# Performance work log

Measured on AMD Instinct MI355X. Metric: run time of the kernel, lower is better.

## Reference

```python
import jax, jax.numpy as jnp
import numpy as np

# ---- problem constants (match init_kwargs / input_specs) ----
R = 10          # rand_iter
B = 8           # num examples
NPG = 1024      # nodes per example (equal-sized groups)
M = 512         # centroids per group = fps_ratio(0.5) * NPG
TOL = 1e-3
MAX_ITER = 300
SCORE_NORM = 1  # L1 scoring


def setup_inputs() -> dict:
    key = jax.random.key(0)
    pos = jax.random.normal(key, (B * NPG, 3), dtype=jnp.float32)
    batch = (jnp.arange(B * NPG) // NPG).astype(jnp.int32)  # sorted example ids
    return {"pos": pos, "batch": batch}


def _fps(p, start):
    """Farthest point sampling on one group. p: [n,3] -> indices [M].
    torch_cluster.fps uses a random start; randomness across the R replicas
    comes from the start index."""
    n = p.shape[0]
    mind = jnp.full((n,), jnp.inf, dtype=p.dtype)

    def step(carry, _):
        mind, last = carry
        d = jnp.sum((p - p[last]) ** 2, axis=-1)     # [n]
        mind = jnp.minimum(mind, d)
        nxt = jnp.argmax(mind).astype(last.dtype)
        return (mind, nxt), last

    (_, _), idx = jax.lax.scan(step, (mind, start), None, length=M)
    return idx  # [M]


def _assign_update(p, c):
    """One k-means step for all groups. p: [g,n,3], c: [g,m,3].
    nearest-centroid assign (within group == within example) + scatter-mean
    update; empty clusters keep their old centroid (mask logic in torch src)."""
    p2 = jnp.sum(p * p, axis=-1)                                 # [g,n]
    c2 = jnp.sum(c * c, axis=-1)                                 # [g,m]
    d2 = p2[:, :, None] - 2.0 * jnp.einsum('gnd,gmd->gnm', p, c) + c2[:, None, :]
    cls = jnp.argmin(d2, axis=-1)                                # [g,n]
    seg = jax.vmap(lambda x, i: jax.ops.segment_sum(x, i, num_segments=M))
    sums = seg(p, cls)                                           # [g,m,3]
    cnts = seg(jnp.ones(p.shape[:2], p.dtype), cls)[..., None]   # [g,m,1]
    newc = jnp.where(cnts > 0, sums / jnp.maximum(cnts, 1.0), c)
    return newc, cls


def reference(pos, batch):
    # replicate data R times (SymmetricKMeans big_pos / big_batch)
    p = pos.reshape(B, NPG, 3)
    big = jnp.broadcast_to(p[None], (R, B, NPG, 3)).reshape(R * B, NPG, 3)

    # FPS init with a different random start per replica-group
    starts = jax.random.randint(jax.random.key(1), (R * B,), 0, NPG)
    idx = jax.vmap(_fps)(big, starts)                            # [g,M]
    cents = jnp.take_along_axis(big, idx[..., None], axis=1)     # [g,M,3]

    # k-means loop with convergence check (KMeans.forward)
    def cond(st):
        c, cls, done, i = st
        return (~done) & (i < MAX_ITER)

    def body(st):
        c, cls, done, i = st
        newc, cls = _assign_update(big, c)
        done = jnp.all(jnp.linalg.norm(c - newc, axis=-1) < TOL)
        return (newc, cls, done, i + 1)

    cls0 = jnp.zeros((R * B, NPG), jnp.int32)
    c, cls, _, _ = jax.lax.while_loop(
        cond, body, (cents, cls0, jnp.array(False), jnp.int32(0)))

    # score: L1 distance to assigned centroid, summed per example (score_norm=1)
    cvec = jnp.take_along_axis(c, cls[..., None], axis=1)        # [g,n,3]
    scores = jnp.sum(jnp.abs(big - cvec), axis=(-1, -2)).reshape(R, B)

    classification = cls.reshape(R, B * NPG)                     # per-group labels
    return classification, c, scores
```

## Files before the change

### kernel.cpp

```cpp
#include <hip/hip_runtime.h>
#include <math.h>


#define NGRP   80
#define NPTS   1024
#define NCTR   512
#define MAXIT  300
#define NTHR   1024
#define RING   64
#define LEAD   48
#define OUT_CENT  81920
#define OUT_SCORE 204800

typedef float v2f __attribute__((ext_vector_type(2)));
static __device__ __forceinline__ v2f mk2(float a, float b) {
  v2f r; r.x = a; r.y = b; return r;
}

__device__ float4   g_cent[NGRP * NCTR];
__device__ int      g_rcls[RING][NGRP * NPTS];
__device__ float4   g_rcent[RING][NGRP * NCTR];
__device__ unsigned g_conv32[MAXIT][32];
__device__ unsigned g_T[32];
__device__ unsigned g_water[32];

__device__ __forceinline__ void tf2x32(unsigned k0, unsigned k1,
                                       unsigned x0, unsigned x1,
                                       unsigned &o0, unsigned &o1) {
  unsigned ks2 = k0 ^ k1 ^ 0x1BD11BDAu;
#define RND(r) { x0 += x1; x1 = (x1 << (r)) | (x1 >> (32 - (r))); x1 ^= x0; }
  x0 += k0; x1 += k1;
  RND(13) RND(15) RND(26) RND(6)
  x0 += k1;  x1 += ks2 + 1u;
  RND(17) RND(29) RND(16) RND(24)
  x0 += ks2; x1 += k0 + 2u;
  RND(13) RND(15) RND(26) RND(6)
  x0 += k0;  x1 += k1 + 3u;
  RND(17) RND(29) RND(16) RND(24)
  x0 += k1;  x1 += ks2 + 4u;
  RND(13) RND(15) RND(26) RND(6)
  x0 += ks2; x1 += k0 + 5u;
#undef RND
  o0 = x0; o1 = x1;
}

#define DPP_MAXF(CTRL) asm volatile("s_nop 1\n\tv_max_f32 %0, %0, %0 " CTRL \
                                    : "+v"(bv));
#define DPP_MINU(CTRL) asm volatile("s_nop 1\n\tv_min_u32 %0, %0, %0 " CTRL \
                                    : "+v"(ci));

__device__ __forceinline__ int wave_iscan(int x) {
  x += __builtin_amdgcn_update_dpp(0, x, 0x111, 0xF, 0xF, true);
  x += __builtin_amdgcn_update_dpp(0, x, 0x112, 0xF, 0xF, true);
  x += __builtin_amdgcn_update_dpp(0, x, 0x114, 0xF, 0xF, true);
  x += __builtin_amdgcn_update_dpp(0, x, 0x118, 0xF, 0xF, true);
  x += __builtin_amdgcn_update_dpp(0, x, 0x142, 0xA, 0xF, true);
  x += __builtin_amdgcn_update_dpp(0, x, 0x143, 0xC, 0xF, true);
  return x;
}

__device__ __forceinline__ void conv_scan(unsigned w, bool &closed, bool &allc) {
  unsigned hz = 0u; bool ac = true;
#pragma unroll
  for (int i = 0; i < 20; ++i) {
    unsigned d = __hip_atomic_load(&g_conv32[w][i], __ATOMIC_RELAXED,
                                   __HIP_MEMORY_SCOPE_AGENT);
    hz |= (d - 0x01010101u) & ~d & 0x80808080u;
    ac = ac && (d == 0x02020202u);
  }
  closed = (hz == 0u); allc = ac;
}

__global__ __launch_bounds__(64) void fps_kernel(const float *__restrict__ pos) {
  const int g = blockIdx.x, t = threadIdx.x;
  const int e = g & 7;
  __shared__ float4 sp4[NPTS];
  {
    const int gid = g * 64 + t, stride = NGRP * 64;
    for (int k = gid; k < MAXIT * 32; k += stride) g_conv32[0][k] = 0u;
    if (gid == 0) { g_T[0] = 0u; g_water[0] = 0u; }
  }
  unsigned s0, s1, o0, o1;
  tf2x32(0u, 1u, 0u, 1u, s0, s1);
  tf2x32(s0, s1, 0u, (unsigned)g, o0, o1);
  int last = (int)((o0 ^ o1) & 1023u);

  const float *p = pos + (size_t)e * NPTS * 3;
  v2f xp[8], yp[8], zp[8], mdp[8];
#pragma unroll
  for (int q = 0; q < 8; ++q) {
    int n0 = (2 * q) * 64 + t, n1 = (2 * q + 1) * 64 + t;
    xp[q] = mk2(p[n0 * 3 + 0], p[n1 * 3 + 0]);
    yp[q] = mk2(p[n0 * 3 + 1], p[n1 * 3 + 1]);
    zp[q] = mk2(p[n0 * 3 + 2], p[n1 * 3 + 2]);
    sp4[n0] = make_float4(xp[q].x, yp[q].x, zp[q].x, 0.f);
    sp4[n1] = make_float4(xp[q].y, yp[q].y, zp[q].y, 0.f);
    mdp[q] = mk2(__int_as_float(0x7f800000), __int_as_float(0x7f800000));
  }
  __syncthreads();
  for (int j = 0; j < NCTR; ++j) {
    const float4 L = sp4[last];
    if (t == 0) {
      float c2 = __fadd_rn(__fadd_rn(__fmul_rn(L.x, L.x), __fmul_rn(L.y, L.y)),
                           __fmul_rn(L.z, L.z));
      g_cent[(size_t)g * NCTR + j] = make_float4(L.x, L.y, L.z, c2);
    }
    {
#pragma clang fp contract(off)
      const v2f lx2 = mk2(L.x, L.x), ly2 = mk2(L.y, L.y), lz2 = mk2(L.z, L.z);
#pragma unroll
      for (int q = 0; q < 8; ++q) {
        v2f dx = xp[q] - lx2, dy = yp[q] - ly2, dz = zp[q] - lz2;
        v2f d = (dx * dx + dy * dy) + dz * dz;
        mdp[q] = __builtin_elementwise_min(mdp[q], d);
      }
    }
    v2f m01 = __builtin_elementwise_max(mdp[0], mdp[1]);
    v2f m23 = __builtin_elementwise_max(mdp[2], mdp[3]);
    v2f m45 = __builtin_elementwise_max(mdp[4], mdp[5]);
    v2f m67 = __builtin_elementwise_max(mdp[6], mdp[7]);
    v2f m03 = __builtin_elementwise_max(m01, m23);
    v2f m47 = __builtin_elementwise_max(m45, m67);
    v2f m07 = __builtin_elementwise_max(m03, m47);
    float bv = fmaxf(m07.x, m07.y);
    DPP_MAXF("row_ror:1")
    DPP_MAXF("row_ror:2")
    DPP_MAXF("row_ror:4")
    DPP_MAXF("row_ror:8")
    DPP_MAXF("row_bcast:15 row_mask:0xa")
    DPP_MAXF("row_bcast:31 row_mask:0xc")
    asm volatile("s_nop 1");
    const float gmax = __int_as_float(
        __builtin_amdgcn_readlane(__float_as_int(bv), 63));

    unsigned cd[16];
#pragma unroll
    for (int k = 0; k < 16; ++k) {
      const float mv = (k & 1) ? mdp[k >> 1].y : mdp[k >> 1].x;
      cd[k] = (mv == gmax) ? (unsigned)(k * 64 + t) : 0x7fffffffu;
    }
#pragma unroll
    for (int s = 8; s >= 1; s >>= 1)
#pragma unroll
      for (int i = 0; i < s; ++i) cd[i] = cd[i] < cd[i + s] ? cd[i] : cd[i + s];
    unsigned ci = cd[0];
    DPP_MINU("row_ror:1")
    DPP_MINU("row_ror:2")
    DPP_MINU("row_ror:4")
    DPP_MINU("row_ror:8")
    DPP_MINU("row_bcast:15 row_mask:0xa")
    DPP_MINU("row_bcast:31 row_mask:0xc")
    asm volatile("s_nop 1");
    last = (int)__builtin_amdgcn_readlane((int)ci, 63);
  }
}

__global__ __launch_bounds__(NTHR) void kmeans_kernel(
    const float *__restrict__ pos, float *__restrict__ out) {
  const int g = blockIdx.x, t = threadIdx.x;
  const int e = g & 7;
  const int lane = t & 63, wv = t >> 6;

  __shared__ float  scp[NCTR / 2][8];
  __shared__ float  spx[NPTS], spy[NPTS], spz[NPTS];
  __shared__ int    slab[NPTS];
  __shared__ int    cnt[NCTR], offs[NCTR];
  __shared__ int    idx[NPTS];
  __shared__ float  redf[16];
  __shared__ double redd[4];
  __shared__ int    swtot[8];
  __shared__ unsigned s_ctl;

  const int cc7 = t & 127, cbid = (t >> 7) & 3;
  const int cq = cc7 + (cbid >> 1) * 128, cs = cbid & 1;

  {
    const float *gp = pos + (size_t)e * NPTS * 3;
    spx[t] = gp[t * 3 + 0]; spy[t] = gp[t * 3 + 1]; spz[t] = gp[t * 3 + 2];
    if (t < NCTR) {
      float4 cc = g_cent[(size_t)g * NCTR + t];
      scp[cq][0 + cs] = cc.x; scp[cq][2 + cs] = cc.y;
      scp[cq][4 + cs] = cc.z; scp[cq][6 + cs] = cc.w;
    }
    if (t == 0) s_ctl = 0u;
  }
  __syncthreads();

  const float px = spx[t], py = spy[t], pz = spz[t];
  const float p2 = __fadd_rn(__fadd_rn(__fmul_rn(px, px), __fmul_rn(py, py)),
                             __fmul_rn(pz, pz));
  const v2f px2 = mk2(px, px), py2 = mk2(py, py), pz2 = mk2(pz, pz);
  const v2f p22 = mk2(p2, p2), two2 = mk2(2.0f, 2.0f);

  int done_sT = -1;
  for (int it = 0; it < MAXIT; ++it) {
    float best0 = __int_as_float(0x7f800000), best1 = best0,
          best2 = best0, best3 = best0;
    int im0 = 0, im1 = 0, im2 = 0, im3 = 0;
    {
#pragma clang fp contract(off)
#pragma unroll 2
      for (int m = 0; m < NCTR / 4; ++m) {
        const float4 lo0 = *(const float4 *)&scp[m][0];
        const float4 hi0 = *(const float4 *)&scp[m][4];
        const float4 lo1 = *(const float4 *)&scp[m + 128][0];
        const float4 hi1 = *(const float4 *)&scp[m + 128][4];
        v2f t0 = px2 * mk2(lo0.x, lo0.y);
        t0 = __builtin_elementwise_fma(py2, mk2(lo0.z, lo0.w), t0);
        t0 = __builtin_elementwise_fma(pz2, mk2(hi0.x, hi0.y), t0);
        v2f dA = (p22 - two2 * t0) + mk2(hi0.z, hi0.w);
        v2f t1 = px2 * mk2(lo1.x, lo1.y);
        t1 = __builtin_elementwise_fma(py2, mk2(lo1.z, lo1.w), t1);
        t1 = __builtin_elementwise_fma(pz2, mk2(hi1.x, hi1.y), t1);
        v2f dB = (p22 - two2 * t1) + mk2(hi1.z, hi1.w);
        float d0 = dA.x, d1 = dA.y, d2 = dB.x, d3 = dB.y;
        if (d0 < best0) { best0 = d0; im0 = m; }
        if (d1 < best1) { best1 = d1; im1 = m; }
        if (d2 < best2) { best2 = d2; im2 = m; }
        if (d3 < best3) { best3 = d3; im3 = m; }
      }
    }
    float best = best0; int bm = im0;
    if (best1 < best) { best = best1; bm = 128 + im1; }
    if (best2 < best) { best = best2; bm = 256 + im2; }
    if (best3 < best) { best = best3; bm = 384 + im3; }
    const int slot = it & (RING - 1);
    g_rcls[slot][(size_t)g * NPTS + t] = bm;
    slab[t] = bm;
    if (t < NCTR) cnt[t] = 0;
    __syncthreads();

    {
      const unsigned tv = s_ctl;
      if (tv != 0u && (int)tv <= it) {
        done_sT = (int)tv - 1;
        break;
      }
    }

    atomicAdd(&cnt[slab[t]], 1);
    __syncthreads();
    int sc = 0;
    if (t < NCTR) {
      sc = wave_iscan(cnt[t]);
      if (lane == 63) swtot[wv] = sc;
    }
    __syncthreads();
    if (t < NCTR) {
      int pre = 0;
#pragma unroll
      for (int w = 0; w < 8; ++w) pre += (w < wv) ? swtot[w] : 0;
      offs[t] = sc + pre;
      cnt[t] = 0;
    }
    __syncthreads();
    {
      int c0 = slab[t]; int sl0 = atomicAdd(&cnt[c0], 1);
      idx[(c0 ? offs[c0 - 1] : 0) + sl0] = t;
    }
    __syncthreads();
    float mx = 0.0f;
    if (t < NCTR) {
      const int c = t;
      const int base = c ? offs[c - 1] : 0;
      const int kk = offs[c] - base;
      for (int i = base + 1; i < base + kk; ++i) {
        int v = idx[i], j = i - 1;
        while (j >= base && idx[j] > v) { idx[j + 1] = idx[j]; --j; }
        idx[j + 1] = v;
      }
      float4 oldc;
      oldc.x = scp[cq][0 + cs]; oldc.y = scp[cq][2 + cs];
      oldc.z = scp[cq][4 + cs]; oldc.w = scp[cq][6 + cs];
      float nx, ny, nz;
      if (kk > 0) {
        float sxx = 0.f, syy = 0.f, szz = 0.f;
        for (int i = 0; i < kk; ++i) {
          int n2 = idx[base + i];
          sxx = __fadd_rn(sxx, spx[n2]);
          syy = __fadd_rn(syy, spy[n2]);
          szz = __fadd_rn(szz, spz[n2]);
        }
        float fc = (float)kk;
        nx = __fdiv_rn(sxx, fc); ny = __fdiv_rn(syy, fc); nz = __fdiv_rn(szz, fc);
      } else { nx = oldc.x; ny = oldc.y; nz = oldc.z; }
      float dx = __fsub_rn(oldc.x, nx), dy = __fsub_rn(oldc.y, ny),
            dz = __fsub_rn(oldc.z, nz);
      float nr = __fsqrt_rn(__fadd_rn(__fadd_rn(__fmul_rn(dx, dx), __fmul_rn(dy, dy)),
                                      __fmul_rn(dz, dz)));
      mx = nr;
      float c2v2 = __fadd_rn(__fadd_rn(__fmul_rn(nx, nx), __fmul_rn(ny, ny)),
                             __fmul_rn(nz, nz));
      scp[cq][0 + cs] = nx; scp[cq][2 + cs] = ny;
      scp[cq][4 + cs] = nz; scp[cq][6 + cs] = c2v2;
      g_rcent[slot][(size_t)g * NCTR + t] =
          make_float4(nx, ny, nz, c2v2);
    }
    for (int off = 32; off; off >>= 1) {
      float o = __shfl_down(mx, off, 64);
      if (o > mx) mx = o;
    }
    if (lane == 0) redf[wv] = mx;
    __syncthreads();

    if (t == 0) {
      unsigned Tl = __hip_atomic_load(&g_T[0], __ATOMIC_RELAXED, __HIP_MEMORY_SCOPE_AGENT);
      if (Tl == 0u) {
        float bmx = fmaxf(fmaxf(fmaxf(redf[0], redf[1]), fmaxf(redf[2], redf[3])),
                          fmaxf(fmaxf(redf[4], redf[5]), fmaxf(redf[6], redf[7])));
        unsigned char cv = (bmx < 1e-3f) ? (unsigned char)2 : (unsigned char)1;
        __hip_atomic_store((unsigned char *)&g_conv32[it][0] + g, cv,
                           __ATOMIC_RELAXED, __HIP_MEMORY_SCOPE_AGENT);
        if (g == 0) {
          unsigned w = __hip_atomic_load(&g_water[0], __ATOMIC_RELAXED,
                                         __HIP_MEMORY_SCOPE_AGENT);
          const unsigned w0 = w;
          while (w <= (unsigned)it) {
            bool closed, allc; conv_scan(w, closed, allc);
            if (!closed) break;
            if (allc) {
              Tl = w + 1u;
              __hip_atomic_store(&g_T[0], Tl, __ATOMIC_RELAXED, __HIP_MEMORY_SCOPE_AGENT);
              ++w; break;
            }
            ++w;
          }
          if (w != w0)
            __hip_atomic_store(&g_water[0], w, __ATOMIC_RELAXED, __HIP_MEMORY_SCOPE_AGENT);
        }
        if (Tl == 0u)
          Tl = __hip_atomic_load(&g_T[0], __ATOMIC_RELAXED, __HIP_MEMORY_SCOPE_AGENT);
      }
      s_ctl = Tl;
      if (Tl == 0u && it + 1 >= LEAD) {
        long long guard = 0;
        for (;;) {
          unsigned wv2 = __hip_atomic_load(&g_water[0], __ATOMIC_RELAXED,
                                           __HIP_MEMORY_SCOPE_AGENT);
          if ((it + 1) - (int)wv2 < LEAD) break;
          if (__hip_atomic_load(&g_T[0], __ATOMIC_RELAXED, __HIP_MEMORY_SCOPE_AGENT))
            break;
          if (g == 0) {
            bool closed, allc; conv_scan(wv2, closed, allc);
            if (closed) {
              if (allc)
                __hip_atomic_store(&g_T[0], wv2 + 1u, __ATOMIC_RELAXED,
                                   __HIP_MEMORY_SCOPE_AGENT);
              __hip_atomic_store(&g_water[0], wv2 + 1u, __ATOMIC_RELAXED,
                                 __HIP_MEMORY_SCOPE_AGENT);
              continue;
            }
          }
          __builtin_amdgcn_s_sleep(4);
          if (++guard > (1ll << 22)) break;
        }
      }
    }
  }

  if (done_sT < 0) {
    if (t == 0) {
      if (g == 0) {
        unsigned w = __hip_atomic_load(&g_water[0], __ATOMIC_RELAXED,
                                       __HIP_MEMORY_SCOPE_AGENT);
        long long guard = 0;
        while (w < (unsigned)MAXIT &&
               __hip_atomic_load(&g_T[0], __ATOMIC_RELAXED,
                                 __HIP_MEMORY_SCOPE_AGENT) == 0u) {
          bool closed, allc; conv_scan(w, closed, allc);
          if (closed) {
            if (allc)
              __hip_atomic_store(&g_T[0], w + 1u, __ATOMIC_RELAXED,
                                 __HIP_MEMORY_SCOPE_AGENT);
            ++w;
            __hip_atomic_store(&g_water[0], w, __ATOMIC_RELAXED,
                               __HIP_MEMORY_SCOPE_AGENT);
          } else {
            __builtin_amdgcn_s_sleep(4);
            if (++guard > (1ll << 22)) break;
          }
        }
        __hip_atomic_store(&g_water[0], (unsigned)MAXIT, __ATOMIC_RELAXED,
                           __HIP_MEMORY_SCOPE_AGENT);
      }
      unsigned Tl = 0; long long guard = 0;
      for (;;) {
        Tl = __hip_atomic_load(&g_T[0], __ATOMIC_RELAXED, __HIP_MEMORY_SCOPE_AGENT);
        if (Tl) break;
        if (__hip_atomic_load(&g_water[0], __ATOMIC_RELAXED,
                              __HIP_MEMORY_SCOPE_AGENT) >= (unsigned)MAXIT) {
          Tl = __hip_atomic_load(&g_T[0], __ATOMIC_RELAXED, __HIP_MEMORY_SCOPE_AGENT);
          break;
        }
        __builtin_amdgcn_s_sleep(4);
        if (++guard > (1ll << 24)) break;
      }
      s_ctl = Tl;
    }
    __syncthreads();
    done_sT = s_ctl ? (int)s_ctl - 1 : (MAXIT - 1);
  }

  const int sT = done_sT;
  const int slot = sT & (RING - 1);
  out[(size_t)g * NPTS + t] =
      (float)g_rcls[slot][(size_t)g * NPTS + t];
  if (t < NCTR) {
    float4 cc = g_rcent[slot][(size_t)g * NCTR + t];
    float *o = out + OUT_CENT + ((size_t)g * NCTR + t) * 3;
    o[0] = cc.x; o[1] = cc.y; o[2] = cc.z;
  }
  if (t < 256) {
    double s = 0.0;
    for (int k = 0; k < 4; ++k) {
      int nn = k * 256 + t;
      int c = g_rcls[slot][(size_t)g * NPTS + nn];
      float4 c4 = g_rcent[slot][(size_t)g * NCTR + c];
      s += (double)fabsf(__fsub_rn(spx[nn], c4.x)) +
           (double)fabsf(__fsub_rn(spy[nn], c4.y)) +
           (double)fabsf(__fsub_rn(spz[nn], c4.z));
    }
    for (int off = 32; off; off >>= 1) s += __shfl_down(s, off, 64);
    if (lane == 0) redd[wv] = s;
  }
  __syncthreads();
  if (t == 0) out[OUT_SCORE + g] = (float)(redd[0] + redd[1] + redd[2] + redd[3]);
}

extern "C" void kernel_launch(void *const *d_in, const int *in_sizes, int n_in,
                              void *d_out, int out_size, void *d_ws, size_t ws_size,
                              hipStream_t stream) {
  const float *pos = (const float *)d_in[0];
  float *out = (float *)d_out;
  (void)d_ws; (void)ws_size; (void)in_sizes; (void)n_in; (void)out_size;

  fps_kernel<<<NGRP, 64, 0, stream>>>(pos);
  kmeans_kernel<<<NGRP, NTHR, 0, stream>>>(pos, out);
}
```

Baseline: 589.1 us.

## Use readlane/ballot in FPS argmax and packed min in k-means assignment

The FPS kernel stops staging points in shared memory and fetches the chosen point's coordinates from registers with readlane through a switch on its index. The argmax step now finishes the max with four readlanes instead of cross-row DPP, and finds the first index with a per-register ballot plus count-trailing-zeros instead of a DPP min-reduction. The k-means assignment loop keeps running best distances in packed 2-wide vectors updated with elementwise min and selects. This aims to cut latency on the serial 512-step FPS chain and the inner assignment loop, at the cost of a 16-way branch per step and 16 ballots per step.

```diff
diff --git a/kernel.cpp b/kernel.cpp
--- a/kernel.cpp
+++ b/kernel.cpp
@@ -46,8 +46,6 @@
 
 #define DPP_MAXF(CTRL) asm volatile("s_nop 1\n\tv_max_f32 %0, %0, %0 " CTRL \
                                     : "+v"(bv));
-#define DPP_MINU(CTRL) asm volatile("s_nop 1\n\tv_min_u32 %0, %0, %0 " CTRL \
-                                    : "+v"(ci));
 
 __device__ __forceinline__ int wave_iscan(int x) {
   x += __builtin_amdgcn_update_dpp(0, x, 0x111, 0xF, 0xF, true);
@@ -74,7 +72,6 @@
 __global__ __launch_bounds__(64) void fps_kernel(const float *__restrict__ pos) {
   const int g = blockIdx.x, t = threadIdx.x;
   const int e = g & 7;
-  __shared__ float4 sp4[NPTS];
   {
     const int gid = g * 64 + t, stride = NGRP * 64;
     for (int k = gid; k < MAXIT * 32; k += stride) g_conv32[0][k] = 0u;
@@ -93,21 +90,31 @@
     xp[q] = mk2(p[n0 * 3 + 0], p[n1 * 3 + 0]);
     yp[q] = mk2(p[n0 * 3 + 1], p[n1 * 3 + 1]);
     zp[q] = mk2(p[n0 * 3 + 2], p[n1 * 3 + 2]);
-    sp4[n0] = make_float4(xp[q].x, yp[q].x, zp[q].x, 0.f);
-    sp4[n1] = make_float4(xp[q].y, yp[q].y, zp[q].y, 0.f);
     mdp[q] = mk2(__int_as_float(0x7f800000), __int_as_float(0x7f800000));
   }
-  __syncthreads();
+
+#define RLF(V) __int_as_float(__builtin_amdgcn_readlane(__float_as_int(V), ln))
+#define FCASE(K, Q, H) case K: lx = RLF(xp[Q].H); ly = RLF(yp[Q].H); \
+                               lz = RLF(zp[Q].H); break;
+
   for (int j = 0; j < NCTR; ++j) {
-    const float4 L = sp4[last];
+    const int kq = last >> 6, ln = last & 63;
+    float lx, ly, lz;
+    switch (kq) {
+      FCASE(0, 0, x)  FCASE(1, 0, y)  FCASE(2, 1, x)  FCASE(3, 1, y)
+      FCASE(4, 2, x)  FCASE(5, 2, y)  FCASE(6, 3, x)  FCASE(7, 3, y)
+      FCASE(8, 4, x)  FCASE(9, 4, y)  FCASE(10, 5, x) FCASE(11, 5, y)
+      FCASE(12, 6, x) FCASE(13, 6, y) FCASE(14, 7, x)
+      default: lx = RLF(xp[7].y); ly = RLF(yp[7].y); lz = RLF(zp[7].y); break;
+    }
     if (t == 0) {
-      float c2 = __fadd_rn(__fadd_rn(__fmul_rn(L.x, L.x), __fmul_rn(L.y, L.y)),
-                           __fmul_rn(L.z, L.z));
-      g_cent[(size_t)g * NCTR + j] = make_float4(L.x, L.y, L.z, c2);
+      float c2 = __fadd_rn(__fadd_rn(__fmul_rn(lx, lx), __fmul_rn(ly, ly)),
+                           __fmul_rn(lz, lz));
+      g_cent[(size_t)g * NCTR + j] = make_float4(lx, ly, lz, c2);
     }
     {
 #pragma clang fp contract(off)
-      const v2f lx2 = mk2(L.x, L.x), ly2 = mk2(L.y, L.y), lz2 = mk2(L.z, L.z);
+      const v2f lx2 = mk2(lx, lx), ly2 = mk2(ly, ly), lz2 = mk2(lz, lz);
 #pragma unroll
       for (int q = 0; q < 8; ++q) {
         v2f dx = xp[q] - lx2, dy = yp[q] - ly2, dz = zp[q] - lz2;
@@ -127,32 +134,24 @@
     DPP_MAXF("row_ror:2")
     DPP_MAXF("row_ror:4")
     DPP_MAXF("row_ror:8")
-    DPP_MAXF("row_bcast:15 row_mask:0xa")
-    DPP_MAXF("row_bcast:31 row_mask:0xc")
     asm volatile("s_nop 1");
-    const float gmax = __int_as_float(
-        __builtin_amdgcn_readlane(__float_as_int(bv), 63));
-
-    unsigned cd[16];
+    const float r0  = __int_as_float(__builtin_amdgcn_readlane(__float_as_int(bv), 0));
+    const float r16 = __int_as_float(__builtin_amdgcn_readlane(__float_as_int(bv), 16));
+    const float r32 = __int_as_float(__builtin_amdgcn_readlane(__float_as_int(bv), 32));
+    const float r48 = __int_as_float(__builtin_amdgcn_readlane(__float_as_int(bv), 48));
+    const float gmax = fmaxf(fmaxf(r0, r16), fmaxf(r32, r48));
+
+    unsigned long long mb = 0ull; int kb = 0;
 #pragma unroll
-    for (int k = 0; k < 16; ++k) {
-      const float mv = (k & 1) ? mdp[k >> 1].y : mdp[k >> 1].x;
-      cd[k] = (mv == gmax) ? (unsigned)(k * 64 + t) : 0x7fffffffu;
-    }
-#pragma unroll
-    for (int s = 8; s >= 1; s >>= 1)
-#pragma unroll
-      for (int i = 0; i < s; ++i) cd[i] = cd[i] < cd[i + s] ? cd[i] : cd[i + s];
-    unsigned ci = cd[0];
-    DPP_MINU("row_ror:1")
-    DPP_MINU("row_ror:2")
-    DPP_MINU("row_ror:4")
-    DPP_MINU("row_ror:8")
-    DPP_MINU("row_bcast:15 row_mask:0xa")
-    DPP_MINU("row_bcast:31 row_mask:0xc")
-    asm volatile("s_nop 1");
-    last = (int)__builtin_amdgcn_readlane((int)ci, 63);
-  }
+    for (int kk = 15; kk >= 0; --kk) {
+      const float mv = (kk & 1) ? mdp[kk >> 1].y : mdp[kk >> 1].x;
+      const unsigned long long mk = __ballot(mv == gmax);
+      if (mk) { mb = mk; kb = kk; }
+    }
+    last = kb * 64 + (int)__builtin_ctzll(mb);
+  }
+#undef FCASE
+#undef RLF
 }
 
 __global__ __launch_bounds__(NTHR) void kmeans_kernel(
@@ -194,8 +193,8 @@
 
   int done_sT = -1;
   for (int it = 0; it < MAXIT; ++it) {
-    float best0 = __int_as_float(0x7f800000), best1 = best0,
-          best2 = best0, best3 = best0;
+    v2f bestA = mk2(__int_as_float(0x7f800000), __int_as_float(0x7f800000));
+    v2f bestB = bestA;
     int im0 = 0, im1 = 0, im2 = 0, im3 = 0;
     {
 #pragma clang fp contract(off)
@@ -213,17 +212,18 @@
         t1 = __builtin_elementwise_fma(py2, mk2(lo1.z, lo1.w), t1);
         t1 = __builtin_elementwise_fma(pz2, mk2(hi1.x, hi1.y), t1);
         v2f dB = (p22 - two2 * t1) + mk2(hi1.z, hi1.w);
-        float d0 = dA.x, d1 = dA.y, d2 = dB.x, d3 = dB.y;
-        if (d0 < best0) { best0 = d0; im0 = m; }
-        if (d1 < best1) { best1 = d1; im1 = m; }
-        if (d2 < best2) { best2 = d2; im2 = m; }
-        if (d3 < best3) { best3 = d3; im3 = m; }
-      }
-    }
-    float best = best0; int bm = im0;
-    if (best1 < best) { best = best1; bm = 128 + im1; }
-    if (best2 < best) { best = best2; bm = 256 + im2; }
-    if (best3 < best) { best = best3; bm = 384 + im3; }
+        const bool c0 = dA.x < bestA.x, c1 = dA.y < bestA.y;
+        const bool c2 = dB.x < bestB.x, c3 = dB.y < bestB.y;
+        bestA = __builtin_elementwise_min(bestA, dA);
+        bestB = __builtin_elementwise_min(bestB, dB);
+        im0 = c0 ? m : im0; im1 = c1 ? m : im1;
+        im2 = c2 ? m : im2; im3 = c3 ? m : im3;
+      }
+    }
+    float best = bestA.x; int bm = im0;
+    if (bestA.y < best) { best = bestA.y; bm = 128 + im1; }
+    if (bestB.x < best) { best = bestB.x; bm = 256 + im2; }
+    if (bestB.y < best) { best = bestB.y; bm = 384 + im3; }
     const int slot = it & (RING - 1);
     g_rcls[slot][(size_t)g * NPTS + t] = bm;
     slab[t] = bm;
```

Result: slower. 713.5 us (+21.1%).
